# Performance work log

Hardware: AMD Instinct MI355X
Metric: run time of the kernel (lower is better)

Reference implementation:

```python
import jax, jax.numpy as jnp
import numpy as np

N, D = 65536, 64            # flattened batch, state dim (size_in)
G, K = 4, 512               # number of gammas, components per gamma


def setup_inputs() -> dict:
    key = jax.random.key(0)
    k1, k2 = jax.random.split(key)
    states = jax.random.normal(k1, (N, D), dtype=jnp.float32)
    centers = jax.random.normal(k2, (G, K, D), dtype=jnp.float32)  # RBF centers, one bank per gamma
    gammas = jnp.array([0.5, 1.0, 2.0, 5.0], dtype=jnp.float32)
    return {"states": states, "centers": centers, "gammas": gammas}


def reference(states, centers, gammas):
    # states: [N, D]; centers: [G, K, D]; gammas: [G]
    x2 = jnp.sum(states * states, axis=-1)            # [N]
    c2 = jnp.sum(centers * centers, axis=-1)          # [G, K]
    xc = jnp.einsum('nd,gkd->gnk', states, centers)   # [G, N, K]
    d2 = x2[None, :, None] + c2[:, None, :] - 2.0 * xc  # [G, N, K]
    d2 = jnp.maximum(d2, 0.0)
    feats = jnp.exp(-gammas[:, None, None] * d2)      # [G, N, K]
    # concatenate per-gamma feature banks along feature dim -> [N, G*K]
    out = jnp.moveaxis(feats, 0, 1).reshape(states.shape[0], -1)
    return out
```

## Files before the change

### kernel.cpp

```cpp
#include <hip/hip_runtime.h>
#include <math.h>

#define N_TOT 65536
#define D_DIM 64
#define G_NUM 4
#define K_NUM 512

#define BM 128
#define BN 128
#define LDS_PAD 4
#define LDW (BM + LDS_PAD)

__global__ void rowsq64_kernel(const float* __restrict__ in,
                               float* __restrict__ out, int nrows) {
    int gtid = blockIdx.x * blockDim.x + threadIdx.x;
    int row  = gtid >> 6;
    int lane = threadIdx.x & 63;
    if (row >= nrows) return;
    float v = in[(size_t)row * D_DIM + lane];
    float s = v * v;
    #pragma unroll
    for (int off = 32; off > 0; off >>= 1)
        s += __shfl_xor(s, off, 64);
    if (lane == 0) out[row] = s;
}

__global__ __launch_bounds__(256, 2)
void rbf_gemm_kernel(const float* __restrict__ states,
                     const float* __restrict__ centers,
                     const float* __restrict__ gammas,
                     const float* __restrict__ x2,
                     const float* __restrict__ c2,
                     float* __restrict__ out)
{
    __shared__ float As[D_DIM][LDW];
    __shared__ float Bs[D_DIM][LDW];

    const int n0 = blockIdx.x * BM;
    const int k0 = blockIdx.y * BN;
    const int g  = blockIdx.z;
    const int tid = threadIdx.x;

    {
        const int r = tid & 15;
        const int c = (tid >> 4) << 2;
        const float* ap = states  + ((size_t)(n0 + r)) * D_DIM + c;
        const float* bp = centers + ((size_t)g * K_NUM + (size_t)(k0 + r)) * D_DIM + c;
        #pragma unroll
        for (int i = 0; i < 8; ++i) {
            float4 av = *(const float4*)(ap + (size_t)(16 * i) * D_DIM);
            float4 bv = *(const float4*)(bp + (size_t)(16 * i) * D_DIM);
            int rr = r + 16 * i;
            As[c + 0][rr] = av.x; As[c + 1][rr] = av.y;
            As[c + 2][rr] = av.z; As[c + 3][rr] = av.w;
            Bs[c + 0][rr] = bv.x; Bs[c + 1][rr] = bv.y;
            Bs[c + 2][rr] = bv.z; Bs[c + 3][rr] = bv.w;
        }
    }
    __syncthreads();

    const int tx = tid & 15;
    const int ty = tid >> 4;

    float acc[8][8];
    #pragma unroll
    for (int i = 0; i < 8; ++i)
        #pragma unroll
        for (int j = 0; j < 8; ++j) acc[i][j] = 0.0f;

    #pragma unroll 8
    for (int d = 0; d < D_DIM; ++d) {
        float4 a0 = *(const float4*)&As[d][ty * 4];
        float4 a1 = *(const float4*)&As[d][64 + ty * 4];
        float4 b0 = *(const float4*)&Bs[d][tx * 4];
        float4 b1 = *(const float4*)&Bs[d][64 + tx * 4];
        float a[8] = {a0.x, a0.y, a0.z, a0.w, a1.x, a1.y, a1.z, a1.w};
        float b[8] = {b0.x, b0.y, b0.z, b0.w, b1.x, b1.y, b1.z, b1.w};
        #pragma unroll
        for (int i = 0; i < 8; ++i)
            #pragma unroll
            for (int j = 0; j < 8; ++j)
                acc[i][j] = fmaf(a[i], b[j], acc[i][j]);
    }

    const float gamma = gammas[g];

    float x2v[8], c2v[8];
    #pragma unroll
    for (int i = 0; i < 8; ++i) {
        int m = 4 * ty + (i & 3) + ((i >> 2) << 6);
        x2v[i] = x2[n0 + m];
        int k = 4 * tx + (i & 3) + ((i >> 2) << 6);
        c2v[i] = c2[g * K_NUM + k0 + k];
    }

    const size_t row_stride = (size_t)(G_NUM * K_NUM);
    #pragma unroll
    for (int i = 0; i < 8; ++i) {
        int m = 4 * ty + (i & 3) + ((i >> 2) << 6);
        float* orow = out + (size_t)(n0 + m) * row_stride + (size_t)g * K_NUM + k0;
        float vals[8];
        #pragma unroll
        for (int j = 0; j < 8; ++j) {
            float d2 = x2v[i] + c2v[j] - 2.0f * acc[i][j];
            d2 = fmaxf(d2, 0.0f);
            vals[j] = __expf(-gamma * d2);
        }
        float4 o0 = make_float4(vals[0], vals[1], vals[2], vals[3]);
        float4 o1 = make_float4(vals[4], vals[5], vals[6], vals[7]);
        *(float4*)(orow + 4 * tx)      = o0;
        *(float4*)(orow + 64 + 4 * tx) = o1;
    }
}

extern "C" void kernel_launch(void* const* d_in, const int* in_sizes, int n_in,
                              void* d_out, int out_size, void* d_ws, size_t ws_size,
                              hipStream_t stream) {
    const float* states  = (const float*)d_in[0];
    const float* centers = (const float*)d_in[1];
    const float* gammas  = (const float*)d_in[2];
    float* out = (float*)d_out;

    float* x2 = (float*)d_ws;
    float* c2 = x2 + N_TOT;

    {
        int threads = 256;
        int blocks_x2 = (N_TOT * 64) / threads;
        int blocks_c2 = (G_NUM * K_NUM * 64) / threads;
        rowsq64_kernel<<<blocks_x2, threads, 0, stream>>>(states, x2, N_TOT);
        rowsq64_kernel<<<blocks_c2, threads, 0, stream>>>(centers, c2, G_NUM * K_NUM);
    }

    dim3 grid(N_TOT / BM, K_NUM / BN, G_NUM);
    rbf_gemm_kernel<<<grid, 256, 0, stream>>>(states, centers, gammas, x2, c2, out);
}
```

Measured before the change: 676.7 us.

## Replace FP32 FMA GEMM with split-bf16 MFMA using swizzled LDS tiles

The scalar FP32 outer-product loop is replaced by bf16 MFMA instructions (16x16x32). Each fp32 operand is split into a high and a low bf16 part, and three MFMA products are accumulated to keep close to fp32 accuracy. Tiles are stored in a XOR-swizzled LDS layout to avoid bank conflicts. The output store changes from float4 vector writes to scalar writes following the MFMA accumulator layout. That store pattern could cut write efficiency on a kernel that is dominated by its 537 MB of output writes.

```diff
diff --git a/kernel.cpp b/kernel.cpp
--- a/kernel.cpp
+++ b/kernel.cpp
@@ -5,11 +5,28 @@
 #define D_DIM 64
 #define G_NUM 4
 #define K_NUM 512
-
 #define BM 128
 #define BN 128
-#define LDS_PAD 4
-#define LDW (BM + LDS_PAD)
+
+typedef __attribute__((ext_vector_type(4))) float  f32x4;
+typedef __attribute__((ext_vector_type(8))) short  short8;
+
+__device__ __forceinline__ unsigned int f2u(float x)        { return __builtin_bit_cast(unsigned int, x); }
+__device__ __forceinline__ float        u2f(unsigned int x) { return __builtin_bit_cast(float, x); }
+
+__device__ __forceinline__ unsigned int bf_rne(float x) {
+    unsigned int u = f2u(x);
+    return (u + 0x7FFFu + ((u >> 16) & 1u)) >> 16;
+}
+
+__device__ __forceinline__ int swz(int row, int byteInRow) {
+    return (row << 7) + (byteInRow ^ ((row & 7) << 4));
+}
+
+#define AHI_OFF 0
+#define ALO_OFF 16384
+#define BHI_OFF 32768
+#define BLO_OFF 49152
 
 __global__ void rowsq64_kernel(const float* __restrict__ in,
                                float* __restrict__ out, int nrows) {
@@ -26,90 +43,126 @@
 }
 
 __global__ __launch_bounds__(256, 2)
-void rbf_gemm_kernel(const float* __restrict__ states,
+void rbf_mfma_kernel(const float* __restrict__ states,
                      const float* __restrict__ centers,
                      const float* __restrict__ gammas,
                      const float* __restrict__ x2,
                      const float* __restrict__ c2,
                      float* __restrict__ out)
 {
-    __shared__ float As[D_DIM][LDW];
-    __shared__ float Bs[D_DIM][LDW];
+    __shared__ __align__(16) unsigned char lds[65536];
 
-    const int n0 = blockIdx.x * BM;
-    const int k0 = blockIdx.y * BN;
-    const int g  = blockIdx.z;
     const int tid = threadIdx.x;
+    const int n0  = blockIdx.x * BM;
+    const int k0  = blockIdx.y * BN;
+    const int g   = blockIdx.z;
 
     {
-        const int r = tid & 15;
-        const int c = (tid >> 4) << 2;
-        const float* ap = states  + ((size_t)(n0 + r)) * D_DIM + c;
-        const float* bp = centers + ((size_t)g * K_NUM + (size_t)(k0 + r)) * D_DIM + c;
+        const int r0 = tid >> 4;
+        const int cc = tid & 15;
         #pragma unroll
         for (int i = 0; i < 8; ++i) {
-            float4 av = *(const float4*)(ap + (size_t)(16 * i) * D_DIM);
-            float4 bv = *(const float4*)(bp + (size_t)(16 * i) * D_DIM);
-            int rr = r + 16 * i;
-            As[c + 0][rr] = av.x; As[c + 1][rr] = av.y;
-            As[c + 2][rr] = av.z; As[c + 3][rr] = av.w;
-            Bs[c + 0][rr] = bv.x; Bs[c + 1][rr] = bv.y;
-            Bs[c + 2][rr] = bv.z; Bs[c + 3][rr] = bv.w;
+            const int row = r0 + 16 * i;
+            const float4 av = *(const float4*)(states  + (size_t)(n0 + row) * D_DIM + 4 * cc);
+            const float4 bv = *(const float4*)(centers + ((size_t)g * K_NUM + (size_t)(k0 + row)) * D_DIM + 4 * cc);
+            const int wb = swz(row, 8 * cc);
+
+            {
+                unsigned h0 = f2u(av.x) & 0xFFFF0000u, h1 = f2u(av.y) & 0xFFFF0000u;
+                unsigned h2 = f2u(av.z) & 0xFFFF0000u, h3 = f2u(av.w) & 0xFFFF0000u;
+                uint2 hi = make_uint2((h0 >> 16) | h1, (h2 >> 16) | h3);
+                uint2 lo = make_uint2(bf_rne(av.x - u2f(h0)) | (bf_rne(av.y - u2f(h1)) << 16),
+                                      bf_rne(av.z - u2f(h2)) | (bf_rne(av.w - u2f(h3)) << 16));
+                *(uint2*)(lds + AHI_OFF + wb) = hi;
+                *(uint2*)(lds + ALO_OFF + wb) = lo;
+            }
+            {
+                unsigned h0 = f2u(bv.x) & 0xFFFF0000u, h1 = f2u(bv.y) & 0xFFFF0000u;
+                unsigned h2 = f2u(bv.z) & 0xFFFF0000u, h3 = f2u(bv.w) & 0xFFFF0000u;
+                uint2 hi = make_uint2((h0 >> 16) | h1, (h2 >> 16) | h3);
+                uint2 lo = make_uint2(bf_rne(bv.x - u2f(h0)) | (bf_rne(bv.y - u2f(h1)) << 16),
+                                      bf_rne(bv.z - u2f(h2)) | (bf_rne(bv.w - u2f(h3)) << 16));
+                *(uint2*)(lds + BHI_OFF + wb) = hi;
+                *(uint2*)(lds + BLO_OFF + wb) = lo;
+            }
         }
     }
     __syncthreads();
 
-    const int tx = tid & 15;
-    const int ty = tid >> 4;
+    const int lane = tid & 63;
+    const int w    = tid >> 6;
+    const int wr   = w >> 1;
+    const int wc   = w & 1;
+    const int fr   = lane & 15;
+    const int q    = lane >> 4;
 
-    float acc[8][8];
+    short8 ahi[4][2], alo[4][2];
     #pragma unroll
-    for (int i = 0; i < 8; ++i)
+    for (int ms = 0; ms < 4; ++ms) {
+        const int row = wr * 64 + ms * 16 + fr;
         #pragma unroll
-        for (int j = 0; j < 8; ++j) acc[i][j] = 0.0f;
+        for (int h = 0; h < 2; ++h) {
+            const int off = swz(row, 64 * h + 16 * q);
+            ahi[ms][h] = *(const short8*)(lds + AHI_OFF + off);
+            alo[ms][h] = *(const short8*)(lds + ALO_OFF + off);
+        }
+    }
 
-    #pragma unroll 8
-    for (int d = 0; d < D_DIM; ++d) {
-        float4 a0 = *(const float4*)&As[d][ty * 4];
-        float4 a1 = *(const float4*)&As[d][64 + ty * 4];
-        float4 b0 = *(const float4*)&Bs[d][tx * 4];
-        float4 b1 = *(const float4*)&Bs[d][64 + tx * 4];
-        float a[8] = {a0.x, a0.y, a0.z, a0.w, a1.x, a1.y, a1.z, a1.w};
-        float b[8] = {b0.x, b0.y, b0.z, b0.w, b1.x, b1.y, b1.z, b1.w};
+    f32x4 acc[4][4];
+    #pragma unroll
+    for (int ms = 0; ms < 4; ++ms)
         #pragma unroll
-        for (int i = 0; i < 8; ++i)
+        for (int ns = 0; ns < 4; ++ns)
+            acc[ms][ns] = (f32x4){0.f, 0.f, 0.f, 0.f};
+
+    #pragma unroll
+    for (int ns = 0; ns < 4; ++ns) {
+        const int rowb = wc * 64 + ns * 16 + fr;
+        short8 bhi[2], blo[2];
+        #pragma unroll
+        for (int h = 0; h < 2; ++h) {
+            const int off = swz(rowb, 64 * h + 16 * q);
+            bhi[h] = *(const short8*)(lds + BHI_OFF + off);
+            blo[h] = *(const short8*)(lds + BLO_OFF + off);
+        }
+        #pragma unroll
+        for (int ms = 0; ms < 4; ++ms) {
             #pragma unroll
-            for (int j = 0; j < 8; ++j)
-                acc[i][j] = fmaf(a[i], b[j], acc[i][j]);
+            for (int h = 0; h < 2; ++h) {
+                acc[ms][ns] = __builtin_amdgcn_mfma_f32_16x16x32_bf16(ahi[ms][h], bhi[h], acc[ms][ns], 0, 0, 0);
+                acc[ms][ns] = __builtin_amdgcn_mfma_f32_16x16x32_bf16(ahi[ms][h], blo[h], acc[ms][ns], 0, 0, 0);
+                acc[ms][ns] = __builtin_amdgcn_mfma_f32_16x16x32_bf16(alo[ms][h], bhi[h], acc[ms][ns], 0, 0, 0);
+            }
+        }
     }
 
     const float gamma = gammas[g];
 
-    float x2v[8], c2v[8];
+    float x2v[4][4];
     #pragma unroll
-    for (int i = 0; i < 8; ++i) {
-        int m = 4 * ty + (i & 3) + ((i >> 2) << 6);
-        x2v[i] = x2[n0 + m];
-        int k = 4 * tx + (i & 3) + ((i >> 2) << 6);
-        c2v[i] = c2[g * K_NUM + k0 + k];
-    }
+    for (int ms = 0; ms < 4; ++ms)
+        #pragma unroll
+        for (int r = 0; r < 4; ++r)
+            x2v[ms][r] = x2[n0 + wr * 64 + ms * 16 + 4 * q + r];
 
-    const size_t row_stride = (size_t)(G_NUM * K_NUM);
+    float c2v[4];
     #pragma unroll
-    for (int i = 0; i < 8; ++i) {
-        int m = 4 * ty + (i & 3) + ((i >> 2) << 6);
-        float* orow = out + (size_t)(n0 + m) * row_stride + (size_t)g * K_NUM + k0;
-        float vals[8];
+    for (int ns = 0; ns < 4; ++ns)
+        c2v[ns] = c2[g * K_NUM + k0 + wc * 64 + ns * 16 + fr];
+
+    #pragma unroll
+    for (int ms = 0; ms < 4; ++ms) {
         #pragma unroll
-        for (int j = 0; j < 8; ++j) {
-            float d2 = x2v[i] + c2v[j] - 2.0f * acc[i][j];
-            d2 = fmaxf(d2, 0.0f);
-            vals[j] = __expf(-gamma * d2);
+        for (int ns = 0; ns < 4; ++ns) {
+            const size_t col = (size_t)g * K_NUM + k0 + wc * 64 + ns * 16 + fr;
+            #pragma unroll
+            for (int r = 0; r < 4; ++r) {
+                const int rown = n0 + wr * 64 + ms * 16 + 4 * q + r;
+                float d2 = x2v[ms][r] + c2v[ns] - 2.0f * acc[ms][ns][r];
+                d2 = fmaxf(d2, 0.0f);
+                out[(size_t)rown * (G_NUM * K_NUM) + col] = __expf(-gamma * d2);
+            }
         }
-        float4 o0 = make_float4(vals[0], vals[1], vals[2], vals[3]);
-        float4 o1 = make_float4(vals[4], vals[5], vals[6], vals[7]);
-        *(float4*)(orow + 4 * tx)      = o0;
-        *(float4*)(orow + 64 + 4 * tx) = o1;
     }
 }
 
@@ -133,5 +186,5 @@
     }
 
     dim3 grid(N_TOT / BM, K_NUM / BN, G_NUM);
-    rbf_gemm_kernel<<<grid, 256, 0, stream>>>(states, centers, gammas, x2, c2, out);
+    rbf_mfma_kernel<<<grid, 256, 0, stream>>>(states, centers, gammas, x2, c2, out);
 }
```

New measurement: 598.2 us. 11.6% less time.
